# Performance work log

Measured on AMD Instinct MI355X. Metric: run time of the kernel, lower is better.

The kernel has to match this reference:

```python
import jax, jax.numpy as jnp
import numpy as np

GAMMA = 2
EPS = 1e-8


def setup_inputs() -> dict:
    key = jax.random.key(0)
    kx, kw = jax.random.split(key)
    B, C, D, W, H = 4, 256, 16, 16, 16
    x = jax.random.normal(kx, (B, C, D, W, H), dtype=jnp.float32)
    # Conv3d(chan, chan, kernel_size=1) == per-voxel linear: weight (C_out, C_in), bias (C_out,)
    Wt = jax.random.normal(kw, (C, C), dtype=jnp.float32) * 0.02
    b = jnp.zeros((C,), dtype=jnp.float32)
    return {"x": x, "W": Wt, "b": b}


def reference(x, W, b):
    B, C, D, Wd, H = x.shape
    N = D * Wd * H
    xf = x.reshape(B, C, N)                                  # b c n
    # torch cosine_similarity(dim=1): dot / max(|xi|*|xj|, eps)
    norm = jnp.linalg.norm(xf, axis=1, keepdims=True)        # b 1 n
    xn = xf / jnp.maximum(norm, EPS)
    sim = jnp.einsum('bcn,bcm->bnm', xn, xn)                 # b n n (cosine)
    sim = jax.nn.relu(sim) ** GAMMA
    # transform_net: 1x1x1 conv = channel-mixing GEMM per voxel
    t = jnp.einsum('oc,bcm->bom', W, xf) + b[None, :, None]  # b c m
    out = jnp.einsum('bnm,bcm->bcn', sim, t)                 # b c n
    return out.reshape(B, C, D, Wd, H)
```

## Files before the change

### kernel.cpp

```cpp
#include <hip/hip_runtime.h>
#include <hip/hip_bf16.h>


typedef unsigned short u16;
typedef __attribute__((ext_vector_type(8))) short short8;
typedef __attribute__((ext_vector_type(4))) float f32x4;

#define MFMA16(a, b, c) __builtin_amdgcn_mfma_f32_16x16x32_bf16((a), (b), (c), 0, 0, 0)

__device__ __forceinline__ u16 f2bf(float f) {
    union { float f; unsigned u; } v; v.f = f;
    unsigned u = v.u;
    u += 0x7fffu + ((u >> 16) & 1u);
    return (u16)(u >> 16);
}

__device__ __forceinline__ unsigned cvtpk(float lo, float hi) {
    unsigned r;
    asm("v_cvt_pk_bf16_f32 %0, %1, %2" : "=v"(r) : "v"(lo), "v"(hi));
    return r;
}

__global__ __launch_bounds__(256) void k_prep2(const float* __restrict__ x,
                                               const float* __restrict__ W,
                                               const float* __restrict__ bias,
                                               u16* __restrict__ xff,
                                               u16* __restrict__ tbf) {
    __shared__ float xs[256][65];
    __shared__ float part[4][64];
    __shared__ float rs_s[64];
    __shared__ float nrm_s[64];
    __shared__ __align__(16) u16 xfrag[32][512];
    __shared__ u16 lds_t[256][72];

    int bid = blockIdx.x;
    int b = bid >> 6, nt = bid & 63, n0 = nt << 6;
    int tid = threadIdx.x;
    int wid = tid >> 6, lane = tid & 63, lg = lane >> 4, lr = lane & 15;

    int rowg = tid >> 4, l16 = tid & 15;
    const float* xb = x + ((size_t)b << 20) + n0;
#pragma unroll
    for (int s = 0; s < 16; ++s) {
        int row = (s << 4) + rowg;
        float4 v = *(const float4*)(xb + (size_t)row * 4096 + (l16 << 2));
        xs[row][(l16 << 2) + 0] = v.x;
        xs[row][(l16 << 2) + 1] = v.y;
        xs[row][(l16 << 2) + 2] = v.z;
        xs[row][(l16 << 2) + 3] = v.w;
    }
    __syncthreads();
    int q2 = tid >> 6, nl = tid & 63;
    float ss = 0.f;
#pragma unroll 16
    for (int c = 0; c < 64; ++c) {
        float v = xs[(q2 << 6) + c][nl];
        ss += v * v;
    }
    part[q2][nl] = ss;
    __syncthreads();
    if (tid < 64) {
        float t = part[0][tid] + part[1][tid] + part[2][tid] + part[3][tid];
        float nr = sqrtf(t);
        nrm_s[tid] = nr;
        rs_s[tid] = 1.0f / fmaxf(nr, 1e-8f);
    }
    __syncthreads();

    u16* xo = xff + ((size_t)b << 20) + ((size_t)nt << 14);
#pragma unroll
    for (int s = 0; s < 8; ++s) {
        int w2 = (s << 2) + (tid >> 6);
        int tl = ((w2 & 3) << 4) + (tid & 15);
        int c8 = ((w2 >> 2) << 2) + ((tid >> 4) & 3);
        float rsv = rs_s[tl];
        u16 tmp[8];
#pragma unroll
        for (int j = 0; j < 8; ++j)
            tmp[j] = f2bf(xs[(c8 << 3) + j][tl] * rsv);
        int chunk = ((tl >> 4) << 3) + (c8 >> 2);
        *(short8*)(xo + (chunk << 9) + (lane << 3)) = *(const short8*)tmp;
        *(short8*)(&xfrag[chunk][lane << 3]) = *(const short8*)tmp;
    }
    __syncthreads();

    f32x4 zero = {0.f, 0.f, 0.f, 0.f};
    f32x4 acc[4][4];
#pragma unroll
    for (int ci = 0; ci < 4; ++ci)
#pragma unroll
        for (int mj = 0; mj < 4; ++mj) acc[ci][mj] = zero;

#pragma unroll
    for (int kc = 0; kc < 8; ++kc) {
        short8 afr[4], bfr[4];
#pragma unroll
        for (int ci = 0; ci < 4; ++ci) {
            const float* wp = W + (((wid << 6) + (ci << 4) + lr) << 8) + (kc << 5) + (lg << 3);
            float4 w0 = *(const float4*)wp;
            float4 w1 = *(const float4*)(wp + 4);
            union { unsigned u[4]; short8 s; } uw;
            uw.u[0] = cvtpk(w0.x, w0.y);
            uw.u[1] = cvtpk(w0.z, w0.w);
            uw.u[2] = cvtpk(w1.x, w1.y);
            uw.u[3] = cvtpk(w1.z, w1.w);
            afr[ci] = uw.s;
        }
#pragma unroll
        for (int mj = 0; mj < 4; ++mj)
            bfr[mj] = *(const short8*)(&xfrag[(mj << 3) + kc][lane << 3]);
#pragma unroll
        for (int ci = 0; ci < 4; ++ci)
#pragma unroll
            for (int mj = 0; mj < 4; ++mj)
                acc[ci][mj] = MFMA16(afr[ci], bfr[mj], acc[ci][mj]);
    }
    float nv[4];
#pragma unroll
    for (int mj = 0; mj < 4; ++mj)
        nv[mj] = nrm_s[(mj << 4) + lr];
#pragma unroll
    for (int ci = 0; ci < 4; ++ci) {
#pragma unroll
        for (int r = 0; r < 4; ++r) {
            int c = (wid << 6) + (ci << 4) + (lg << 2) + r;
            float bv = bias[c];
#pragma unroll
            for (int mj = 0; mj < 4; ++mj)
                lds_t[c][(mj << 4) + lr] = f2bf(acc[ci][mj][r] * nv[mj] + bv);
        }
    }
    __syncthreads();
    u16* to = tbf + ((size_t)b << 20) + ((size_t)nt << 14);
#pragma unroll
    for (int s = 0; s < 8; ++s) {
        int w2 = (s << 2) + (tid >> 6);
        int cq = w2 >> 3, ci2 = (w2 >> 1) & 3, k2 = w2 & 1;
        short8 v = *(const short8*)(&lds_t[(cq << 6) + (ci2 << 4) + lr][(k2 << 5) + (lg << 3)]);
        *(short8*)(to + (w2 << 9) + (lane << 3)) = v;
    }
}

__global__ __launch_bounds__(512) void k_fused(const u16* __restrict__ xff,
                                               const u16* __restrict__ tbf,
                                               float* __restrict__ out) {
    __shared__ __align__(16) u16 lds_p[8][4096];

#define PBYTE(row, col) ((((row) << 7) + ((col) << 1)) ^ (((row) & 7) << 4))
#define BAR() do { asm volatile("s_waitcnt lgkmcnt(0)" ::: "memory");              \
    __builtin_amdgcn_sched_barrier(0); __builtin_amdgcn_s_barrier();               \
    __builtin_amdgcn_sched_barrier(0); } while (0)

    int bid = blockIdx.x;
    int xcd = bid & 7, grp = bid >> 3;
    int batch = xcd >> 1;
    int nt = grp + 32 * (xcd & 1);
    int n0 = nt << 6;

    const u16* xf_b = xff + ((size_t)batch << 20);
    const u16* tb_f = tbf + ((size_t)batch << 20);
    float* out_b = out + ((size_t)batch << 20);

    int tid = threadIdx.x;
    int wid = tid >> 6, lane = tid & 63, lg = lane >> 4, lr = lane & 15;
    int lane8 = lane << 3;
    f32x4 zero = {0.f, 0.f, 0.f, 0.f};
    char* pbase = (char*)&lds_p[0][0];

    if (wid < 4) {
        int tc = wid;
        int colw = (tc << 4) + lr;
        short8 afrag[4][8];
#pragma unroll
        for (int rt = 0; rt < 4; ++rt)
#pragma unroll
            for (int kc = 0; kc < 8; ++kc)
                afrag[rt][kc] = *(const short8*)(xf_b
                    + ((size_t)((((nt << 2) + rt) << 3) + kc) << 9) + lane8);
        const u16* bb = xf_b + ((size_t)(tc << 3) << 9);
        short8 bfrA[8], bfrB[8];

#define RLDB(BUF, OFF)                                                                     \
        { _Pragma("unroll")                                                                \
          for (int kc = 0; kc < 8; ++kc)                                                   \
              BUF[kc] = *(const short8*)(bb + (OFF) + (kc << 9) + lane8); }

#define SCOMP(BUF, SLOT)                                                                   \
    {                                                                                      \
        f32x4 sac[4];                                                                      \
        _Pragma("unroll") for (int c = 0; c < 4; ++c) sac[c] = zero;                       \
        __builtin_amdgcn_s_setprio(1);                                                     \
        _Pragma("unroll")                                                                  \
        for (int kc = 0; kc < 8; ++kc) {                                                   \
            sac[0] = MFMA16(afrag[0][kc], BUF[kc], sac[0]);                                \
            sac[1] = MFMA16(afrag[1][kc], BUF[kc], sac[1]);                                \
            sac[2] = MFMA16(afrag[2][kc], BUF[kc], sac[2]);                                \
            sac[3] = MFMA16(afrag[3][kc], BUF[kc], sac[3]);                                \
        }                                                                                  \
        __builtin_amdgcn_s_setprio(0);                                                     \
        char* pd = pbase + ((SLOT) << 13);                                                 \
        _Pragma("unroll")                                                                  \
        for (int c = 0; c < 4; ++c) {                                                      \
            float q0 = fmaxf(sac[c][0], 0.f); q0 *= q0;                                    \
            float q1 = fmaxf(sac[c][1], 0.f); q1 *= q1;                                    \
            float q2 = fmaxf(sac[c][2], 0.f); q2 *= q2;                                    \
            float q3 = fmaxf(sac[c][3], 0.f); q3 *= q3;                                    \
            unsigned d01 = cvtpk(q0, q1);                                                  \
            unsigned d23 = cvtpk(q2, q3);                                                  \
            int rw = (lg << 2) + (c << 4);                                                 \
            *(u16*)(pd + PBYTE(rw, colw)) = (u16)d01;                                      \
            *(u16*)(pd + PBYTE(rw + 1, colw)) = (u16)(d01 >> 16);                          \
            *(u16*)(pd + PBYTE(rw + 2, colw)) = (u16)d23;                                  \
            *(u16*)(pd + PBYTE(rw + 3, colw)) = (u16)(d23 >> 16);                          \
        }                                                                                  \
    }

#define PPH_FULL(S0, S1, S2, S3)                                                           \
        SCOMP(bfrA, S0); RLDB(bfrA, 2 * 16384);                                            \
        SCOMP(bfrB, S1); RLDB(bfrB, 3 * 16384);                                            \
        SCOMP(bfrA, S2); RLDB(bfrA, 4 * 16384);                                            \
        SCOMP(bfrB, S3); RLDB(bfrB, 5 * 16384);                                            \
        bb += 4 * 16384; BAR();

        RLDB(bfrA, 0);
        RLDB(bfrB, 16384);
        PPH_FULL(0, 1, 2, 3);
        for (int pp = 0; pp < 7; ++pp) {
            PPH_FULL(4, 5, 6, 7);
            PPH_FULL(0, 1, 2, 3);
        }
        SCOMP(bfrA, 4); RLDB(bfrA, 2 * 16384);
        SCOMP(bfrB, 5); RLDB(bfrB, 3 * 16384);
        SCOMP(bfrA, 6);
        SCOMP(bfrB, 7);
        BAR();
        BAR();
#undef PPH_FULL
#undef SCOMP
#undef RLDB
    } else {
        int cq = wid - 4;
        const u16* tbse = tb_f + ((size_t)(cq << 3) << 9);
        short8 tbcA[4][2], tbcB[4][2];

#define RLDT(TB, OFF)                                                                      \
        { _Pragma("unroll")                                                                \
          for (int ci = 0; ci < 4; ++ci) {                                                 \
              _Pragma("unroll")                                                            \
              for (int k2 = 0; k2 < 2; ++k2)                                               \
                  TB[ci][k2] = *(const short8*)(tbse + (OFF)                               \
                                                + ((((ci << 1) + k2)) << 9) + lane8); } }

#define RDP(PFR, SLOT)                                                                     \
    {                                                                                      \
        char* pc = pbase + ((SLOT) << 13);                                                 \
        _Pragma("unroll")                                                                  \
        for (int nj = 0; nj < 4; ++nj) {                                                   \
            PFR[nj][0] = *(const short8*)(pc + PBYTE((nj << 4) + lr, (lg << 3)));          \
            PFR[nj][1] = *(const short8*)(pc + PBYTE((nj << 4) + lr, 32 + (lg << 3)));     \
        }                                                                                  \
    }

#define OMMA(TC, PFR)                                                                      \
    {                                                                                      \
        __builtin_amdgcn_s_setprio(1);                                                     \
        _Pragma("unroll")                                                                  \
        for (int ci = 0; ci < 4; ++ci) {                                                   \
            _Pragma("unroll")                                                              \
            for (int nj = 0; nj < 4; ++nj) {                                               \
                oacc[ci][nj] = MFMA16(TC[ci][0], PFR[nj][0], oacc[ci][nj]);                \
                oacc[ci][nj] = MFMA16(TC[ci][1], PFR[nj][1], oacc[ci][nj]);                \
            }                                                                              \
        }                                                                                  \
        __builtin_amdgcn_s_setprio(0);                                                     \
    }

#define CPH(S0, S1, S2, S3, MODE)                                                          \
    {                                                                                      \
        short8 pfA[4][2], pfB[4][2];                                                       \
        RDP(pfA, S0); RDP(pfB, S1);                                                        \
        OMMA(tbcA, pfA);                                                                   \
        if ((MODE) >= 1) RLDT(tbcA, 2 * 16384);                                            \
        RDP(pfA, S2);                                                                      \
        OMMA(tbcB, pfB);                                                                   \
        if ((MODE) >= 1) RLDT(tbcB, 3 * 16384);                                            \
        RDP(pfB, S3);                                                                      \
        OMMA(tbcA, pfA);                                                                   \
        if ((MODE) >= 2) RLDT(tbcA, 4 * 16384);                                            \
        OMMA(tbcB, pfB);                                                                   \
        if ((MODE) >= 2) RLDT(tbcB, 5 * 16384);                                            \
        if ((MODE) >= 2) tbse += 4 * 16384;                                                \
        BAR();                                                                             \
    }

        RLDT(tbcA, 0);
        RLDT(tbcB, 16384);
        f32x4 oacc[4][4];
#pragma unroll
        for (int ci = 0; ci < 4; ++ci)
#pragma unroll
            for (int nj = 0; nj < 4; ++nj) oacc[ci][nj] = zero;
        BAR();

        for (int pp = 0; pp < 7; ++pp) {
            CPH(0, 1, 2, 3, 2);
            CPH(4, 5, 6, 7, 2);
        }
        CPH(0, 1, 2, 3, 2);
        CPH(4, 5, 6, 7, 1);
#undef CPH
#undef OMMA
#undef RDP
#undef RLDT

#pragma unroll
        for (int ci = 0; ci < 4; ++ci) {
            int c = (cq << 6) + (ci << 4) + (lg << 2);
#pragma unroll
            for (int nj = 0; nj < 4; ++nj) {
                int n = n0 + (nj << 4) + lr;
                float* op = out_b + (size_t)c * 4096 + n;
#pragma unroll
                for (int r = 0; r < 4; ++r) op[(size_t)r * 4096] = oacc[ci][nj][r];
            }
        }
    }
#undef PBYTE
#undef BAR
}

extern "C" void kernel_launch(void* const* d_in, const int* in_sizes, int n_in,
                              void* d_out, int out_size, void* d_ws, size_t ws_size,
                              hipStream_t stream) {
    const float* x = (const float*)d_in[0];
    const float* W = (const float*)d_in[1];
    const float* bias = (const float*)d_in[2];
    float* out = (float*)d_out;

    char* ws = (char*)d_ws;
    u16* xff = (u16*)ws;
    u16* tbf = (u16*)(ws + ((size_t)8 << 20));

    hipLaunchKernelGGL(k_prep2, dim3(256), dim3(256), 0, stream, x, W, bias, xff, tbf);
    hipLaunchKernelGGL(k_fused, dim3(256), dim3(512), 0, stream, xff, tbf, out);
}
```

Baseline: 81.86 us.

## Split prep kernel into normalization and separate transform GEMM kernel

Splits the fused prep kernel in two. The first kernel normalizes x into bf16 fragments, writes the norms to global memory and pre-converts W into bf16 MFMA fragment layout. A new second kernel runs the channel-mixing GEMM from these global buffers. This lowers per-block LDS use and stops every block from re-converting W from fp32, at the cost of an extra kernel launch and a global round trip for the x fragments and norms.

```diff
diff --git a/kernel.cpp b/kernel.cpp
--- a/kernel.cpp
+++ b/kernel.cpp
@@ -21,22 +21,29 @@
     return r;
 }
 
-__global__ __launch_bounds__(256) void k_prep2(const float* __restrict__ x,
-                                               const float* __restrict__ W,
-                                               const float* __restrict__ bias,
-                                               u16* __restrict__ xff,
-                                               u16* __restrict__ tbf) {
+__global__ __launch_bounds__(256) void k_prep(const float* __restrict__ x,
+                                              const float* __restrict__ W,
+                                              u16* __restrict__ xff,
+                                              u16* __restrict__ Wf,
+                                              float* __restrict__ nrm) {
     __shared__ float xs[256][65];
     __shared__ float part[4][64];
     __shared__ float rs_s[64];
-    __shared__ float nrm_s[64];
-    __shared__ __align__(16) u16 xfrag[32][512];
-    __shared__ u16 lds_t[256][72];
-
     int bid = blockIdx.x;
     int b = bid >> 6, nt = bid & 63, n0 = nt << 6;
     int tid = threadIdx.x;
-    int wid = tid >> 6, lane = tid & 63, lg = lane >> 4, lr = lane & 15;
+
+    if (bid < 32) {
+        int q = (bid << 8) + tid;
+        int lane = q & 63, kc = (q >> 6) & 7, ci = (q >> 9) & 3, wq = q >> 11;
+        int row = (wq << 6) + (ci << 4) + (lane & 15);
+        int col = (kc << 5) + ((lane >> 4) << 3);
+        const float* wp = W + row * 256 + col;
+        u16 tmp[8];
+#pragma unroll
+        for (int j = 0; j < 8; ++j) tmp[j] = f2bf(wp[j]);
+        *(short8*)(Wf + ((size_t)q << 3)) = *(const short8*)tmp;
+    }
 
     int rowg = tid >> 4, l16 = tid & 15;
     const float* xb = x + ((size_t)b << 20) + n0;
@@ -62,12 +69,13 @@
     if (tid < 64) {
         float t = part[0][tid] + part[1][tid] + part[2][tid] + part[3][tid];
         float nr = sqrtf(t);
-        nrm_s[tid] = nr;
+        nrm[(b << 12) + n0 + tid] = nr;
         rs_s[tid] = 1.0f / fmaxf(nr, 1e-8f);
     }
     __syncthreads();
 
     u16* xo = xff + ((size_t)b << 20) + ((size_t)nt << 14);
+    int lane = tid & 63;
 #pragma unroll
     for (int s = 0; s < 8; ++s) {
         int w2 = (s << 2) + (tid >> 6);
@@ -80,9 +88,19 @@
             tmp[j] = f2bf(xs[(c8 << 3) + j][tl] * rsv);
         int chunk = ((tl >> 4) << 3) + (c8 >> 2);
         *(short8*)(xo + (chunk << 9) + (lane << 3)) = *(const short8*)tmp;
-        *(short8*)(&xfrag[chunk][lane << 3]) = *(const short8*)tmp;
-    }
-    __syncthreads();
+    }
+}
+
+__global__ __launch_bounds__(256) void k_tgemm(const u16* __restrict__ Wf,
+                                               const u16* __restrict__ xff,
+                                               const float* __restrict__ bias,
+                                               const float* __restrict__ nrm,
+                                               u16* __restrict__ tbf) {
+    __shared__ u16 lds_t[256][72];
+    int bid = blockIdx.x;
+    int b = bid >> 6, mt = bid & 63;
+    const u16* xf_t = xff + ((size_t)b << 20) + ((size_t)mt << 14);
+    int tid = threadIdx.x, wid = tid >> 6, lane = tid & 63, lg = lane >> 4, lr = lane & 15;
 
     f32x4 zero = {0.f, 0.f, 0.f, 0.f};
     f32x4 acc[4][4];
@@ -95,20 +113,13 @@
     for (int kc = 0; kc < 8; ++kc) {
         short8 afr[4], bfr[4];
 #pragma unroll
-        for (int ci = 0; ci < 4; ++ci) {
-            const float* wp = W + (((wid << 6) + (ci << 4) + lr) << 8) + (kc << 5) + (lg << 3);
-            float4 w0 = *(const float4*)wp;
-            float4 w1 = *(const float4*)(wp + 4);
-            union { unsigned u[4]; short8 s; } uw;
-            uw.u[0] = cvtpk(w0.x, w0.y);
-            uw.u[1] = cvtpk(w0.z, w0.w);
-            uw.u[2] = cvtpk(w1.x, w1.y);
-            uw.u[3] = cvtpk(w1.z, w1.w);
-            afr[ci] = uw.s;
-        }
+        for (int ci = 0; ci < 4; ++ci)
+            afr[ci] = *(const short8*)(Wf + ((size_t)((((wid << 2) + ci) << 3) + kc) << 9)
+                                       + (lane << 3));
 #pragma unroll
         for (int mj = 0; mj < 4; ++mj)
-            bfr[mj] = *(const short8*)(&xfrag[(mj << 3) + kc][lane << 3]);
+            bfr[mj] = *(const short8*)(xf_t + ((size_t)(((mj << 3) + kc)) << 9)
+                                       + (lane << 3));
 #pragma unroll
         for (int ci = 0; ci < 4; ++ci)
 #pragma unroll
@@ -118,7 +129,7 @@
     float nv[4];
 #pragma unroll
     for (int mj = 0; mj < 4; ++mj)
-        nv[mj] = nrm_s[(mj << 4) + lr];
+        nv[mj] = nrm[(b << 12) + (mt << 6) + (mj << 4) + lr];
 #pragma unroll
     for (int ci = 0; ci < 4; ++ci) {
 #pragma unroll
@@ -131,7 +142,7 @@
         }
     }
     __syncthreads();
-    u16* to = tbf + ((size_t)b << 20) + ((size_t)nt << 14);
+    u16* to = tbf + ((size_t)b << 20) + ((size_t)mt << 14);
 #pragma unroll
     for (int s = 0; s < 8; ++s) {
         int w2 = (s << 2) + (tid >> 6);
@@ -340,7 +351,10 @@
     char* ws = (char*)d_ws;
     u16* xff = (u16*)ws;
     u16* tbf = (u16*)(ws + ((size_t)8 << 20));
-
-    hipLaunchKernelGGL(k_prep2, dim3(256), dim3(256), 0, stream, x, W, bias, xff, tbf);
+    u16* Wf = (u16*)(ws + ((size_t)16 << 20));
+    float* nrm = (float*)(ws + ((size_t)16 << 20) + (192u << 10));
+
+    hipLaunchKernelGGL(k_prep, dim3(256), dim3(256), 0, stream, x, W, xff, Wf, nrm);
+    hipLaunchKernelGGL(k_tgemm, dim3(256), dim3(256), 0, stream, Wf, xff, bias, nrm, tbf);
     hipLaunchKernelGGL(k_fused, dim3(256), dim3(512), 0, stream, xff, tbf, out);
 }
```

Result: faster. 76.43 us (median of 2 runs) (-6.6%).
